# Kernel optimization log

Measured on AMD Instinct MI355X. Metric: run time of the kernel, lower is better.

## Reference

```python
import jax, jax.numpy as jnp
import numpy as np

B, P, N, D = 32, 100, 1000, 128
SQRT_D = 11.313708498984761
CLIP = 10.0


def setup_inputs() -> dict:
    key = jax.random.key(0)
    ks = jax.random.split(key, 8)
    s = 1.0 / np.sqrt(D)  # keep k ~ N(0,1) so exp(k) is stable
    return {
        "encoded_nodes": jax.random.normal(ks[0], (B, N, D), jnp.float32),
        "encoded_q1": jax.random.normal(ks[1], (B, P, D), jnp.float32),
        "encoded_last_node": jax.random.normal(ks[2], (B, P, D), jnp.float32),
        "cur_dist": jax.random.uniform(ks[3], (B, P, N), jnp.float32),
        "ninf_mask": jnp.zeros((B, P, N), jnp.float32),
        "log_scale": jnp.ones((1,), jnp.float32),
        "Wq_first": jax.random.normal(ks[4], (D, D), jnp.float32) * s,
        "Wq_last": jax.random.normal(ks[5], (D, D), jnp.float32) * s,
        "Wk": jax.random.normal(ks[6], (D, D), jnp.float32) * s,
        "Wv": jax.random.normal(ks[7], (D, D), jnp.float32) * s,
        "dist_alpha_1": jnp.ones((1,), jnp.float32),
        "AFT_dist_alpha_1": jnp.ones((1,), jnp.float32),
    }


def reference(encoded_nodes, encoded_q1, encoded_last_node, cur_dist, ninf_mask,
              log_scale, Wq_first, Wq_last, Wk, Wv, dist_alpha_1, AFT_dist_alpha_1):
    # set_kv / set_q1 (torch Linear: x @ W.T)
    k = jnp.einsum('bnd,ed->bne', encoded_nodes, Wk)          # [B,N,D]
    v = jnp.einsum('bnd,ed->bne', encoded_nodes, Wv)          # [B,N,D]
    q_first = jnp.einsum('bpd,ed->bpe', encoded_q1, Wq_first) # [B,P,D]
    q_last = jnp.einsum('bpd,ed->bpe', encoded_last_node, Wq_last)
    q = q_first + q_last

    cur_dist_out = -cur_dist                                   # [B,P,N]
    bias_scale = log_scale * AFT_dist_alpha_1 * cur_dist_out + ninf_mask
    ebias = jnp.exp(bias_scale)                                # [B,P,N]
    ek = jnp.exp(k)                                            # [B,N,D]
    num = jnp.einsum('bpn,bnd->bpd', ebias, ek * v)
    den = jnp.einsum('bpn,bnd->bpd', ebias, ek)
    aft_out = jax.nn.sigmoid(q) * (num / den)                  # [B,P,D]

    score = jnp.einsum('bpd,bnd->bpn', aft_out, encoded_nodes) / SQRT_D
    score = score + log_scale * dist_alpha_1 * cur_dist_out
    score = CLIP * jnp.tanh(score) + ninf_mask
    return jax.nn.softmax(score, axis=2)
```

## Files before the change

kernel.cpp:

```cpp
#include <hip/hip_runtime.h>
#include <hip/hip_bf16.h>
#include <math.h>

#define B 32
#define P 100
#define N 1000
#define D 128

constexpr float SQRT_D_INV = 1.0f / 11.313708498984761f;
constexpr float CLIPV = 10.0f;

__device__ __forceinline__ void fma4(float4& a, float s, const float4& b) {
    a.x = fmaf(s, b.x, a.x);
    a.y = fmaf(s, b.y, a.y);
    a.z = fmaf(s, b.z, a.z);
    a.w = fmaf(s, b.w, a.w);
}

__global__ void transpose_w4(const float* __restrict__ Wk,
                             const float* __restrict__ Wv,
                             const float* __restrict__ Wqf,
                             const float* __restrict__ Wql,
                             float* __restrict__ wkT,
                             float* __restrict__ wvT,
                             float* __restrict__ wqfT,
                             float* __restrict__ wqlT) {
    const int e = blockIdx.x;
    const int d = threadIdx.x;
    wkT[e * D + d]  = Wk[d * D + e];
    wvT[e * D + d]  = Wv[d * D + e];
    wqfT[e * D + d] = Wqf[d * D + e];
    wqlT[e * D + d] = Wql[d * D + e];
}

#define TT 64
__global__ __launch_bounds__(256) void transpose_nodes(
        const float* __restrict__ nodes, float* __restrict__ nodesT) {
    __shared__ float sh[TT][D + 1];
    const int ntiles = (N + TT - 1) / TT;
    const int b  = blockIdx.x / ntiles;
    const int n0 = (blockIdx.x % ntiles) * TT;
    const int t = threadIdx.x;
    const int rows = min(TT, N - n0);

    const float4* src = (const float4*)(nodes + ((long)b * N + n0) * D);
    for (int i = t; i < rows * (D / 4); i += 256) {
        int r = i >> 5, c = i & 31;
        float4 v = src[(long)r * (D / 4) + c];
        sh[r][c * 4 + 0] = v.x; sh[r][c * 4 + 1] = v.y;
        sh[r][c * 4 + 2] = v.z; sh[r][c * 4 + 3] = v.w;
    }
    __syncthreads();

    const int nl = t & 63;
    const int eg = t >> 6;
    if (nl < rows) {
        #pragma unroll
        for (int k = 0; k < 32; ++k) {
            int e = eg * 32 + k;
            nodesT[((long)b * D + e) * N + n0 + nl] = sh[nl][e];
        }
    }
}

#define R1 32
__global__ __launch_bounds__(256) void kv_kernel(
        const float* __restrict__ nodes,
        const float* __restrict__ wkT,
        const float* __restrict__ wvT,
        float* __restrict__ ek,
        float* __restrict__ ekv) {
    __shared__ float sh[R1][D];
    const int t = threadIdx.x;
    const int dq = t & 31;
    const int rl = t >> 5;
    const long row0 = (long)blockIdx.x * R1;

    const float4* src = (const float4*)(nodes + row0 * D);
    float4* dst = (float4*)(&sh[0][0]);
    #pragma unroll
    for (int i = 0; i < (R1 * D / 4) / 256; ++i)
        dst[t + i * 256] = src[t + i * 256];
    __syncthreads();

    float4 ka[4], va[4];
    #pragma unroll
    for (int rr = 0; rr < 4; ++rr) {
        ka[rr] = make_float4(0.f, 0.f, 0.f, 0.f);
        va[rr] = make_float4(0.f, 0.f, 0.f, 0.f);
    }

    const float* wkp = wkT + dq * 4;
    const float* wvp = wvT + dq * 4;

    float4 cwk[4], cwv[4];
    #pragma unroll
    for (int ee = 0; ee < 4; ++ee) {
        cwk[ee] = *(const float4*)(wkp + ee * D);
        cwv[ee] = *(const float4*)(wvp + ee * D);
    }

    for (int e0 = 0; e0 < D; e0 += 4) {
        float4 nwk[4], nwv[4];
        if (e0 + 4 < D) {
            #pragma unroll
            for (int ee = 0; ee < 4; ++ee) {
                nwk[ee] = *(const float4*)(wkp + (e0 + 4 + ee) * D);
                nwv[ee] = *(const float4*)(wvp + (e0 + 4 + ee) * D);
            }
        }
        #pragma unroll
        for (int rr = 0; rr < 4; ++rr) {
            float4 s4 = *(const float4*)(&sh[rl * 4 + rr][e0]);
            fma4(ka[rr], s4.x, cwk[0]); fma4(ka[rr], s4.y, cwk[1]);
            fma4(ka[rr], s4.z, cwk[2]); fma4(ka[rr], s4.w, cwk[3]);
            fma4(va[rr], s4.x, cwv[0]); fma4(va[rr], s4.y, cwv[1]);
            fma4(va[rr], s4.z, cwv[2]); fma4(va[rr], s4.w, cwv[3]);
        }
        #pragma unroll
        for (int ee = 0; ee < 4; ++ee) { cwk[ee] = nwk[ee]; cwv[ee] = nwv[ee]; }
    }

    #pragma unroll
    for (int rr = 0; rr < 4; ++rr) {
        long row = row0 + rl * 4 + rr;
        float4 e4;
        e4.x = __expf(ka[rr].x); e4.y = __expf(ka[rr].y);
        e4.z = __expf(ka[rr].z); e4.w = __expf(ka[rr].w);
        float4 ev;
        ev.x = e4.x * va[rr].x; ev.y = e4.y * va[rr].y;
        ev.z = e4.z * va[rr].z; ev.w = e4.w * va[rr].w;
        *(float4*)(ek + row * D + dq * 4) = e4;
        *(float4*)(ekv + row * D + dq * 4) = ev;
    }
}

#define R2 16
__global__ __launch_bounds__(256) void q_kernel(
        const float* __restrict__ q1,
        const float* __restrict__ qlast,
        const float* __restrict__ wqfT,
        const float* __restrict__ wqlT,
        float* __restrict__ qsig) {
    __shared__ float sh1[R2][D];
    __shared__ float sh2[R2][D];
    const int t = threadIdx.x;
    const int dq = t & 31;
    const int rl = t >> 5;
    const long row0 = (long)blockIdx.x * R2;

    const float4* s1 = (const float4*)(q1 + row0 * D);
    const float4* s2 = (const float4*)(qlast + row0 * D);
    float4* d1 = (float4*)(&sh1[0][0]);
    float4* d2 = (float4*)(&sh2[0][0]);
    #pragma unroll
    for (int i = 0; i < (R2 * D / 4) / 256; ++i) {
        d1[t + i * 256] = s1[t + i * 256];
        d2[t + i * 256] = s2[t + i * 256];
    }
    __syncthreads();

    float4 acc[2];
    acc[0] = make_float4(0.f, 0.f, 0.f, 0.f);
    acc[1] = make_float4(0.f, 0.f, 0.f, 0.f);

    const float* wfp = wqfT + dq * 4;
    const float* wlp = wqlT + dq * 4;

    float4 cwf[4], cwl[4];
    #pragma unroll
    for (int ee = 0; ee < 4; ++ee) {
        cwf[ee] = *(const float4*)(wfp + ee * D);
        cwl[ee] = *(const float4*)(wlp + ee * D);
    }

    for (int e0 = 0; e0 < D; e0 += 4) {
        float4 nwf[4], nwl[4];
        if (e0 + 4 < D) {
            #pragma unroll
            for (int ee = 0; ee < 4; ++ee) {
                nwf[ee] = *(const float4*)(wfp + (e0 + 4 + ee) * D);
                nwl[ee] = *(const float4*)(wlp + (e0 + 4 + ee) * D);
            }
        }
        #pragma unroll
        for (int rr = 0; rr < 2; ++rr) {
            float4 a4 = *(const float4*)(&sh1[rl * 2 + rr][e0]);
            float4 b4 = *(const float4*)(&sh2[rl * 2 + rr][e0]);
            fma4(acc[rr], a4.x, cwf[0]); fma4(acc[rr], a4.y, cwf[1]);
            fma4(acc[rr], a4.z, cwf[2]); fma4(acc[rr], a4.w, cwf[3]);
            fma4(acc[rr], b4.x, cwl[0]); fma4(acc[rr], b4.y, cwl[1]);
            fma4(acc[rr], b4.z, cwl[2]); fma4(acc[rr], b4.w, cwl[3]);
        }
        #pragma unroll
        for (int ee = 0; ee < 4; ++ee) { cwf[ee] = nwf[ee]; cwl[ee] = nwl[ee]; }
    }

    #pragma unroll
    for (int rr = 0; rr < 2; ++rr) {
        long row = row0 + rl * 2 + rr;
        float4 s;
        s.x = 1.0f / (1.0f + __expf(-acc[rr].x));
        s.y = 1.0f / (1.0f + __expf(-acc[rr].y));
        s.z = 1.0f / (1.0f + __expf(-acc[rr].z));
        s.w = 1.0f / (1.0f + __expf(-acc[rr].w));
        *(float4*)(qsig + row * D + dq * 4) = s;
    }
}

#define PT 20
__global__ __launch_bounds__(128) void aft_part_kernel(
        const float* __restrict__ cur_dist,
        const float* __restrict__ ninf,
        const float* __restrict__ ek,
        const float* __restrict__ ekv,
        const float* __restrict__ log_scale,
        const float* __restrict__ aft_alpha,
        float* __restrict__ pnum,
        float* __restrict__ pden,
        int NC, int L) {
    __shared__ float eb[128][PT];
    const int t = threadIdx.x;
    const int dq = t & 31;
    const int pl = t >> 5;
    const int c  = blockIdx.x % NC;
    const int pt = (blockIdx.x / NC) % (P / PT);
    const int b  = blockIdx.x / (NC * (P / PT));
    const int p0 = pt * PT;
    const int n_begin = c * L;
    const int n_end = min(N, n_begin + L);
    const float lsA = log_scale[0] * aft_alpha[0];

    float4 num[5], den[5];
    #pragma unroll
    for (int i = 0; i < 5; ++i) {
        num[i] = make_float4(0.f, 0.f, 0.f, 0.f);
        den[i] = make_float4(0.f, 0.f, 0.f, 0.f);
    }

    for (int n0 = n_begin; n0 < n_end; n0 += 128) {
        const int lim = min(128, n_end - n0);
        __syncthreads();
        if (t < lim) {
            int n = n0 + t;
            #pragma unroll
            for (int i = 0; i < PT; ++i) {
                long idx = ((long)b * P + p0 + i) * N + n;
                eb[t][i] = __expf(fmaf(-lsA, cur_dist[idx], ninf[idx]));
            }
        }
        __syncthreads();

        const float* ekb = ek  + ((long)b * N + n0) * D + dq * 4;
        const float* evb = ekv + ((long)b * N + n0) * D + dq * 4;

        float4 cek[4], cev[4];
        #pragma unroll
        for (int jj = 0; jj < 4; ++jj) {
            cek[jj] = *(const float4*)(ekb + (long)jj * D);
            cev[jj] = *(const float4*)(evb + (long)jj * D);
        }

        for (int jb = 0; jb < lim; jb += 4) {
            float4 nek[4], nev[4];
            if (jb + 4 < lim) {
                #pragma unroll
                for (int jj = 0; jj < 4; ++jj) {
                    nek[jj] = *(const float4*)(ekb + (long)(jb + 4 + jj) * D);
                    nev[jj] = *(const float4*)(evb + (long)(jb + 4 + jj) * D);
                }
            }
            #pragma unroll
            for (int jj = 0; jj < 4; ++jj) {
                const int j = jb + jj;
                float4 e4 = *(const float4*)(&eb[j][pl * 4]);
                float es = eb[j][16 + pl];
                fma4(num[0], e4.x, cev[jj]); fma4(den[0], e4.x, cek[jj]);
                fma4(num[1], e4.y, cev[jj]); fma4(den[1], e4.y, cek[jj]);
                fma4(num[2], e4.z, cev[jj]); fma4(den[2], e4.z, cek[jj]);
                fma4(num[3], e4.w, cev[jj]); fma4(den[3], e4.w, cek[jj]);
                fma4(num[4], es,   cev[jj]); fma4(den[4], es,   cek[jj]);
            }
            #pragma unroll
            for (int jj = 0; jj < 4; ++jj) { cek[jj] = nek[jj]; cev[jj] = nev[jj]; }
        }
    }

    #pragma unroll
    for (int r = 0; r < 4; ++r) {
        int p = pl * 4 + r;
        long o = (((long)c * B + b) * P + p0 + p) * D + dq * 4;
        *(float4*)(pnum + o) = num[r];
        *(float4*)(pden + o) = den[r];
    }
    {
        int p = 16 + pl;
        long o = (((long)c * B + b) * P + p0 + p) * D + dq * 4;
        *(float4*)(pnum + o) = num[4];
        *(float4*)(pden + o) = den[4];
    }
}

#define PT2 10
__global__ __launch_bounds__(512) void score_kernel(
        const float* __restrict__ pnum,
        const float* __restrict__ pden,
        const float* __restrict__ qsig,
        const float* __restrict__ nodesT,
        const float* __restrict__ cur_dist,
        const float* __restrict__ ninf,
        const float* __restrict__ log_scale,
        const float* __restrict__ dist_alpha,
        float* __restrict__ out, int NC) {
    __shared__ float sa[PT2][D];
    __shared__ float red[8][PT2];
    __shared__ float bmax[PT2];
    __shared__ float bsum[PT2];
    const int t = threadIdx.x;
    const int wid = t >> 6;
    const int pt = blockIdx.x % (P / PT2);
    const int b  = blockIdx.x / (P / PT2);
    const int p0 = pt * PT2;
    const float lsA = log_scale[0] * dist_alpha[0];
    const long BPD = (long)B * P * D;

    for (int idx = t; idx < PT2 * D; idx += 512) {
        int i = idx >> 7;
        int d = idx & 127;
        long o = ((long)b * P + p0 + i) * D + d;
        float nsum = 0.f, dsum = 0.f;
        for (int c = 0; c < NC; ++c) {
            nsum += pnum[(long)c * BPD + o];
            dsum += pden[(long)c * BPD + o];
        }
        sa[i][d] = qsig[o] * nsum / dsum;
    }
    __syncthreads();

    const int n0 = t * 2;
    const bool act = (n0 < N);
    const int ncl = act ? n0 : 0;
    const float* ntb = nodesT + (long)b * D * N;

    float2 acc[PT2];
    #pragma unroll
    for (int i = 0; i < PT2; ++i) acc[i] = make_float2(0.f, 0.f);

    float2 cx[4];
    #pragma unroll
    for (int ee = 0; ee < 4; ++ee)
        cx[ee] = *(const float2*)(ntb + (long)ee * N + ncl);

    for (int e0 = 0; e0 < D; e0 += 4) {
        float2 nx[4];
        if (e0 + 4 < D) {
            #pragma unroll
            for (int ee = 0; ee < 4; ++ee)
                nx[ee] = *(const float2*)(ntb + (long)(e0 + 4 + ee) * N + ncl);
        }
        #pragma unroll
        for (int i = 0; i < PT2; ++i) {
            float4 a4 = *(const float4*)(&sa[i][e0]);
            acc[i].x = fmaf(cx[0].x, a4.x, acc[i].x);
            acc[i].x = fmaf(cx[1].x, a4.y, acc[i].x);
            acc[i].x = fmaf(cx[2].x, a4.z, acc[i].x);
            acc[i].x = fmaf(cx[3].x, a4.w, acc[i].x);
            acc[i].y = fmaf(cx[0].y, a4.x, acc[i].y);
            acc[i].y = fmaf(cx[1].y, a4.y, acc[i].y);
            acc[i].y = fmaf(cx[2].y, a4.z, acc[i].y);
            acc[i].y = fmaf(cx[3].y, a4.w, acc[i].y);
        }
        #pragma unroll
        for (int ee = 0; ee < 4; ++ee) cx[ee] = nx[ee];
    }

    float2 sc[PT2];
    #pragma unroll
    for (int i = 0; i < PT2; ++i) {
        if (act) {
            long idx = ((long)b * P + p0 + i) * N + n0;
            float2 cd = *(const float2*)(cur_dist + idx);
            float2 nf = *(const float2*)(ninf + idx);
            float sx = fmaf(acc[i].x, SQRT_D_INV, -lsA * cd.x);
            float sy = fmaf(acc[i].y, SQRT_D_INV, -lsA * cd.y);
            float ax = fabsf(sx), ay = fabsf(sy);
            float rx = 1.f - 2.f / (__expf(2.f * ax) + 1.f);
            float ry = 1.f - 2.f / (__expf(2.f * ay) + 1.f);
            sc[i].x = CLIPV * copysignf(rx, sx) + nf.x;
            sc[i].y = CLIPV * copysignf(ry, sy) + nf.y;
        } else {
            sc[i].x = -INFINITY;
            sc[i].y = -INFINITY;
        }
    }

    #pragma unroll
    for (int i = 0; i < PT2; ++i) {
        float m = fmaxf(sc[i].x, sc[i].y);
        #pragma unroll
        for (int o = 1; o < 64; o <<= 1) m = fmaxf(m, __shfl_xor(m, o, 64));
        if ((t & 63) == 0) red[wid][i] = m;
    }
    __syncthreads();
    if (t < PT2) {
        float mm = red[0][t];
        #pragma unroll
        for (int w = 1; w < 8; ++w) mm = fmaxf(mm, red[w][t]);
        bmax[t] = mm;
    }
    __syncthreads();

    float2 ex[PT2];
    #pragma unroll
    for (int i = 0; i < PT2; ++i) {
        float m = bmax[i];
        ex[i].x = (sc[i].x > -1e30f) ? __expf(sc[i].x - m) : 0.f;
        ex[i].y = (sc[i].y > -1e30f) ? __expf(sc[i].y - m) : 0.f;
        float ssum = ex[i].x + ex[i].y;
        #pragma unroll
        for (int o = 1; o < 64; o <<= 1) ssum += __shfl_xor(ssum, o, 64);
        if ((t & 63) == 0) red[wid][i] = ssum;
    }
    __syncthreads();
    if (t < PT2) {
        float ss = red[0][t];
        #pragma unroll
        for (int w = 1; w < 8; ++w) ss += red[w][t];
        bsum[t] = ss;
    }
    __syncthreads();

    #pragma unroll
    for (int i = 0; i < PT2; ++i) {
        if (act) {
            float inv = 1.0f / bsum[i];
            long idx = ((long)b * P + p0 + i) * N + n0;
            *(float2*)(out + idx) = make_float2(ex[i].x * inv, ex[i].y * inv);
        }
    }
}

extern "C" void kernel_launch(void* const* d_in, const int* in_sizes, int n_in,
                              void* d_out, int out_size, void* d_ws, size_t ws_size,
                              hipStream_t stream) {
    const float* nodes      = (const float*)d_in[0];
    const float* q1         = (const float*)d_in[1];
    const float* qlast      = (const float*)d_in[2];
    const float* cur_dist   = (const float*)d_in[3];
    const float* ninf       = (const float*)d_in[4];
    const float* log_scale  = (const float*)d_in[5];
    const float* Wqf        = (const float*)d_in[6];
    const float* Wql        = (const float*)d_in[7];
    const float* Wk         = (const float*)d_in[8];
    const float* Wv         = (const float*)d_in[9];
    const float* dist_alpha = (const float*)d_in[10];
    const float* aft_alpha  = (const float*)d_in[11];
    float* out = (float*)d_out;

    const long BND = (long)B * N * D;
    const long BPD = (long)B * P * D;
    const long W2  = (long)D * D;

    float* ws     = (float*)d_ws;
    float* ek     = ws;
    float* ekv    = ek + BND;
    float* qsig   = ekv + BND;
    float* wkT    = qsig + BPD;
    float* wvT    = wkT + W2;
    float* wqfT   = wvT + W2;
    float* wqlT   = wqfT + W2;
    float* nodesT = wqlT + W2;
    float* pnum   = nodesT + BND;

    long avail = (long)(ws_size / 4) - (3 * BND + BPD + 4 * W2);
    int NC = (int)(avail / (2 * BPD));
    if (NC < 1) NC = 1;
    if (NC > 16) NC = 16;
    int L = (((N + NC - 1) / NC) + 3) & ~3;
    NC = (N + L - 1) / L;
    float* pden = pnum + (long)NC * BPD;

    transpose_w4<<<D, D, 0, stream>>>(Wk, Wv, Wqf, Wql, wkT, wvT, wqfT, wqlT);
    transpose_nodes<<<B * ((N + TT - 1) / TT), 256, 0, stream>>>(nodes, nodesT);
    kv_kernel<<<(B * N) / R1, 256, 0, stream>>>(nodes, wkT, wvT, ek, ekv);
    q_kernel<<<(B * P) / R2, 256, 0, stream>>>(q1, qlast, wqfT, wqlT, qsig);
    aft_part_kernel<<<B * (P / PT) * NC, 128, 0, stream>>>(
        cur_dist, ninf, ek, ekv, log_scale, aft_alpha, pnum, pden, NC, L);
    score_kernel<<<B * (P / PT2), 512, 0, stream>>>(
        pnum, pden, qsig, nodesT, cur_dist, ninf, log_scale, dist_alpha, out, NC);
}
```

Measured before the change: 258.8 us.

## Double-buffer AFT bias tiles with coalesced loads and merge transpose kernels

```diff
diff --git a/kernel.cpp b/kernel.cpp
--- a/kernel.cpp
+++ b/kernel.cpp
@@ -17,30 +17,32 @@
     a.w = fmaf(s, b.w, a.w);
 }
 
-__global__ void transpose_w4(const float* __restrict__ Wk,
-                             const float* __restrict__ Wv,
-                             const float* __restrict__ Wqf,
-                             const float* __restrict__ Wql,
-                             float* __restrict__ wkT,
-                             float* __restrict__ wvT,
-                             float* __restrict__ wqfT,
-                             float* __restrict__ wqlT) {
-    const int e = blockIdx.x;
-    const int d = threadIdx.x;
-    wkT[e * D + d]  = Wk[d * D + e];
-    wvT[e * D + d]  = Wv[d * D + e];
-    wqfT[e * D + d] = Wqf[d * D + e];
-    wqlT[e * D + d] = Wql[d * D + e];
-}
-
 #define TT 64
-__global__ __launch_bounds__(256) void transpose_nodes(
-        const float* __restrict__ nodes, float* __restrict__ nodesT) {
+__global__ __launch_bounds__(256) void prep_kernel(
+        const float* __restrict__ nodes,
+        const float* __restrict__ Wk,  const float* __restrict__ Wv,
+        const float* __restrict__ Wqf, const float* __restrict__ Wql,
+        float* __restrict__ wkT,  float* __restrict__ wvT,
+        float* __restrict__ wqfT, float* __restrict__ wqlT,
+        float* __restrict__ nodesT) {
+    const int t = threadIdx.x;
+    if (blockIdx.x < D) {
+        const int e = blockIdx.x;
+        const int d = t & 127;
+        if ((t >> 7) == 0) {
+            wkT[e * D + d] = Wk[d * D + e];
+            wvT[e * D + d] = Wv[d * D + e];
+        } else {
+            wqfT[e * D + d] = Wqf[d * D + e];
+            wqlT[e * D + d] = Wql[d * D + e];
+        }
+        return;
+    }
     __shared__ float sh[TT][D + 1];
+    const int blk = blockIdx.x - D;
     const int ntiles = (N + TT - 1) / TT;
-    const int b  = blockIdx.x / ntiles;
-    const int n0 = (blockIdx.x % ntiles) * TT;
-    const int t = threadIdx.x;
+    const int b  = blk / ntiles;
+    const int n0 = (blk % ntiles) * TT;
     const int rows = min(TT, N - n0);
 
     const float4* src = (const float4*)(nodes + ((long)b * N + n0) * D);
@@ -209,6 +211,7 @@
 }
 
 #define PT 20
+#define TS 32
 __global__ __launch_bounds__(128) void aft_part_kernel(
         const float* __restrict__ cur_dist,
         const float* __restrict__ ninf,
@@ -219,10 +222,11 @@
         float* __restrict__ pnum,
         float* __restrict__ pden,
         int NC, int L) {
-    __shared__ float eb[128][PT];
+    __shared__ float eb[2][TS][33];
     const int t = threadIdx.x;
     const int dq = t & 31;
     const int pl = t >> 5;
+    const int pl5 = pl * 5;
     const int c  = blockIdx.x % NC;
     const int pt = (blockIdx.x / NC) % (P / PT);
     const int b  = blockIdx.x / (NC * (P / PT));
@@ -238,66 +242,74 @@
         den[i] = make_float4(0.f, 0.f, 0.f, 0.f);
     }
 
-    for (int n0 = n_begin; n0 < n_end; n0 += 128) {
-        const int lim = min(128, n_end - n0);
+    float rv[5];
+    int n0 = n_begin;
+    int ts = min(TS, n_end - n0);
+
+    #pragma unroll
+    for (int k = 0; k < 5; ++k) {
+        int s = t + k * 128;
+        int pp = s >> 5, nl = s & 31;
+        rv[k] = 0.f;
+        if (nl < ts) {
+            long idx = ((long)b * P + p0 + pp) * N + (n0 + nl);
+            rv[k] = fmaf(-lsA, cur_dist[idx], ninf[idx]);
+        }
+    }
+
+    int buf = 0;
+    while (n0 < n_end) {
+        #pragma unroll
+        for (int k = 0; k < 5; ++k) {
+            int s = t + k * 128;
+            int pp = s >> 5, nl = s & 31;
+            if (nl < ts) eb[buf][nl][pp] = __expf(rv[k]);
+        }
         __syncthreads();
-        if (t < lim) {
-            int n = n0 + t;
+
+        const int n0n = n0 + ts;
+        const int tsn = min(TS, n_end - n0n);
+        if (n0n < n_end) {
             #pragma unroll
-            for (int i = 0; i < PT; ++i) {
-                long idx = ((long)b * P + p0 + i) * N + n;
-                eb[t][i] = __expf(fmaf(-lsA, cur_dist[idx], ninf[idx]));
+            for (int k = 0; k < 5; ++k) {
+                int s = t + k * 128;
+                int pp = s >> 5, nl = s & 31;
+                rv[k] = 0.f;
+                if (nl < tsn) {
+                    long idx = ((long)b * P + p0 + pp) * N + (n0n + nl);
+                    rv[k] = fmaf(-lsA, cur_dist[idx], ninf[idx]);
+                }
             }
         }
-        __syncthreads();
 
         const float* ekb = ek  + ((long)b * N + n0) * D + dq * 4;
         const float* evb = ekv + ((long)b * N + n0) * D + dq * 4;
-
-        float4 cek[4], cev[4];
-        #pragma unroll
-        for (int jj = 0; jj < 4; ++jj) {
-            cek[jj] = *(const float4*)(ekb + (long)jj * D);
-            cev[jj] = *(const float4*)(evb + (long)jj * D);
-        }
-
-        for (int jb = 0; jb < lim; jb += 4) {
-            float4 nek[4], nev[4];
-            if (jb + 4 < lim) {
-                #pragma unroll
-                for (int jj = 0; jj < 4; ++jj) {
-                    nek[jj] = *(const float4*)(ekb + (long)(jb + 4 + jj) * D);
-                    nev[jj] = *(const float4*)(evb + (long)(jb + 4 + jj) * D);
-                }
-            }
-            #pragma unroll
-            for (int jj = 0; jj < 4; ++jj) {
-                const int j = jb + jj;
-                float4 e4 = *(const float4*)(&eb[j][pl * 4]);
-                float es = eb[j][16 + pl];
-                fma4(num[0], e4.x, cev[jj]); fma4(den[0], e4.x, cek[jj]);
-                fma4(num[1], e4.y, cev[jj]); fma4(den[1], e4.y, cek[jj]);
-                fma4(num[2], e4.z, cev[jj]); fma4(den[2], e4.z, cek[jj]);
-                fma4(num[3], e4.w, cev[jj]); fma4(den[3], e4.w, cek[jj]);
-                fma4(num[4], es,   cev[jj]); fma4(den[4], es,   cek[jj]);
-            }
-            #pragma unroll
-            for (int jj = 0; jj < 4; ++jj) { cek[jj] = nek[jj]; cev[jj] = nev[jj]; }
-        }
-    }
-
-    #pragma unroll
-    for (int r = 0; r < 4; ++r) {
-        int p = pl * 4 + r;
-        long o = (((long)c * B + b) * P + p0 + p) * D + dq * 4;
+        #pragma unroll 4
+        for (int j = 0; j < ts; ++j) {
+            float4 ekq = *(const float4*)(ekb + (long)j * D);
+            float4 evq = *(const float4*)(evb + (long)j * D);
+            float e0 = eb[buf][j][pl5 + 0];
+            float e1 = eb[buf][j][pl5 + 1];
+            float e2 = eb[buf][j][pl5 + 2];
+            float e3 = eb[buf][j][pl5 + 3];
+            float e4 = eb[buf][j][pl5 + 4];
+            fma4(num[0], e0, evq); fma4(den[0], e0, ekq);
+            fma4(num[1], e1, evq); fma4(den[1], e1, ekq);
+            fma4(num[2], e2, evq); fma4(den[2], e2, ekq);
+            fma4(num[3], e3, evq); fma4(den[3], e3, ekq);
+            fma4(num[4], e4, evq); fma4(den[4], e4, ekq);
+        }
+        buf ^= 1;
+        n0 = n0n;
+        ts = tsn;
+    }
+
+    #pragma unroll
+    for (int r = 0; r < 5; ++r) {
+        int p = p0 + pl5 + r;
+        long o = (((long)c * B + b) * P + p) * D + dq * 4;
         *(float4*)(pnum + o) = num[r];
         *(float4*)(pden + o) = den[r];
-    }
-    {
-        int p = 16 + pl;
-        long o = (((long)c * B + b) * P + p0 + p) * D + dq * 4;
-        *(float4*)(pnum + o) = num[4];
-        *(float4*)(pden + o) = den[4];
     }
 }
 
@@ -475,13 +487,13 @@
     long avail = (long)(ws_size / 4) - (3 * BND + BPD + 4 * W2);
     int NC = (int)(avail / (2 * BPD));
     if (NC < 1) NC = 1;
-    if (NC > 16) NC = 16;
-    int L = (((N + NC - 1) / NC) + 3) & ~3;
+    if (NC > 12) NC = 12;
+    int L = (N + NC - 1) / NC;
     NC = (N + L - 1) / L;
     float* pden = pnum + (long)NC * BPD;
 
-    transpose_w4<<<D, D, 0, stream>>>(Wk, Wv, Wqf, Wql, wkT, wvT, wqfT, wqlT);
-    transpose_nodes<<<B * ((N + TT - 1) / TT), 256, 0, stream>>>(nodes, nodesT);
+    prep_kernel<<<D + B * ((N + TT - 1) / TT), 256, 0, stream>>>(
+        nodes, Wk, Wv, Wqf, Wql, wkT, wvT, wqfT, wqlT, nodesT);
     kv_kernel<<<(B * N) / R1, 256, 0, stream>>>(nodes, wkT, wvT, ek, ekv);
     q_kernel<<<(B * P) / R2, 256, 0, stream>>>(q1, qlast, wqfT, wqlT, qsig);
     aft_part_kernel<<<B * (P / PT) * NC, 128, 0, stream>>>(
```

Result: faster. 250.2 us (-3.3%).
